# Kernel optimization log

Hardware: AMD Instinct MI355X
Metric: run time of the kernel (lower is better)

The kernel has to match this reference:

```python
import jax, jax.numpy as jnp
import numpy as np

N_NODES = 100000
N_EDGES = 1600000
N_GRAPHS = 64
BN_EPS = 1e-5


def setup_inputs() -> dict:
    key = jax.random.key(0)
    ks = jax.random.split(key, 16)
    inp = {
        'x': jax.random.normal(ks[0], (N_NODES, 768), dtype=jnp.float32),
        'edge_index': jax.random.randint(ks[1], (2, N_EDGES), 0, N_NODES, dtype=jnp.int32),
        'batch': jnp.sort(jax.random.randint(ks[2], (N_NODES,), 0, N_GRAPHS, dtype=jnp.int32)),
        'W_in': jax.random.normal(ks[3], (768, 256), dtype=jnp.float32) * 0.02,
        'b_in': jax.random.normal(ks[4], (256,), dtype=jnp.float32) * 0.02,
        'W_g': jax.random.normal(ks[5], (3, 256, 256), dtype=jnp.float32) * 0.05,
        'b_g': jax.random.normal(ks[6], (3, 256), dtype=jnp.float32) * 0.02,
        'bn_gamma': jax.random.uniform(ks[7], (3, 256), dtype=jnp.float32) + 0.5,
        'bn_beta': jax.random.normal(ks[8], (3, 256), dtype=jnp.float32) * 0.02,
        'bn_mean': jax.random.normal(ks[9], (3, 256), dtype=jnp.float32) * 0.02,
        'bn_var': jax.random.uniform(ks[10], (3, 256), dtype=jnp.float32) + 0.5,
        'W1': jax.random.normal(ks[11], (256, 128), dtype=jnp.float32) * 0.06,
        'b1': jax.random.normal(ks[12], (128,), dtype=jnp.float32) * 0.02,
        'W2': jax.random.normal(ks[13], (128, 128), dtype=jnp.float32) * 0.08,
        'b2': jax.random.normal(ks[14], (128,), dtype=jnp.float32) * 0.02,
    }
    return inp


def reference(x, edge_index, batch, W_in, b_in, W_g, b_g, bn_gamma, bn_beta,
              bn_mean, bn_var, W1, b1, W2, b2):
    N = x.shape[0]
    # Add self loops (PyG GCNConv default)
    loop = jnp.arange(N, dtype=edge_index.dtype)
    src = jnp.concatenate([edge_index[0], loop])  # [E+N]
    dst = jnp.concatenate([edge_index[1], loop])
    # Symmetric GCN normalization: deg over dst after self loops
    deg = jax.ops.segment_sum(jnp.ones_like(src, dtype=x.dtype), dst, num_segments=N)
    dinv = jnp.where(deg > 0, jax.lax.rsqrt(deg), 0.0)
    norm = (dinv[src] * dinv[dst])[:, None]  # [E+N, 1]

    # input projection + relu
    h = jax.nn.relu(x @ W_in + b_in)  # [N, 256]

    for i in range(W_g.shape[0]):
        m = h @ W_g[i]                                   # [N, 256]
        agg = jax.ops.segment_sum(m[src] * norm, dst, num_segments=N) + b_g[i]
        # BatchNorm (eval mode, running stats)
        agg = (agg - bn_mean[i]) * (bn_gamma[i] * jax.lax.rsqrt(bn_var[i] + BN_EPS)) + bn_beta[i]
        h = jax.nn.relu(agg)  # dropout is identity in eval

    # global mean pool per graph
    sums = jax.ops.segment_sum(h, batch, num_segments=N_GRAPHS)       # [G, 256]
    cnts = jax.ops.segment_sum(jnp.ones((N,), x.dtype), batch, num_segments=N_GRAPHS)
    g = sums / jnp.maximum(cnts, 1.0)[:, None]

    # output MLP
    out = jax.nn.relu(g @ W1 + b1) @ W2 + b2  # [G, 128]
    return out
```

## Files before the change

### kernel.cpp

```cpp
#include <hip/hip_runtime.h>
#include <hip/hip_fp16.h>

#define HIDDEN 256

using bfrag = __attribute__((ext_vector_type(8))) short;
using facc4 = __attribute__((ext_vector_type(4))) float;

#define BARRIER_LGKM()                                   \
  do {                                                   \
    asm volatile("s_waitcnt lgkmcnt(0)" ::: "memory");   \
    __builtin_amdgcn_s_barrier();                        \
  } while (0)

__device__ inline short bf16_rne(float x) {
  unsigned u = __builtin_bit_cast(unsigned, x);
  unsigned r = u + 0x7FFFu + ((u >> 16) & 1u);
  return (short)(r >> 16);
}
__device__ inline float bf16_to_f(short h) {
  unsigned u = ((unsigned)(unsigned short)h) << 16;
  return __builtin_bit_cast(float, u);
}
__device__ inline float h2f(unsigned short h) {
  return __half2float(__builtin_bit_cast(__half, h));
}
__device__ inline void cvt8(const float4& a, const float4& b, bfrag& hi, bfrag& lo) {
  float av[8] = {a.x, a.y, a.z, a.w, b.x, b.y, b.z, b.w};
#pragma unroll
  for (int i = 0; i < 8; ++i) {
    unsigned u = __builtin_bit_cast(unsigned, av[i]);
    hi[i] = (short)(u >> 16);
    float r = av[i] - __builtin_bit_cast(float, u & 0xFFFF0000u);
    lo[i] = (short)(__builtin_bit_cast(unsigned, r) >> 16);
  }
}

__global__ __launch_bounds__(256) void k_hist(const int* __restrict__ dst,
                                              int* __restrict__ deg, int E) {
  for (int e = blockIdx.x * blockDim.x + threadIdx.x; e < E;
       e += gridDim.x * blockDim.x)
    atomicAdd(&deg[dst[e]], 1);
}

__global__ __launch_bounds__(256) void k_scan_a(const int* __restrict__ deg,
                                                int* __restrict__ bsum, int N) {
  const int t = threadIdx.x, lane = t & 63, w = t >> 6;
  const int idx = blockIdx.x * 256 + t;
  int x = (idx < N) ? deg[idx] : 0;
#pragma unroll
  for (int off = 32; off >= 1; off >>= 1) x += __shfl_xor(x, off);
  __shared__ int ws[4];
  if (lane == 0) ws[w] = x;
  __syncthreads();
  if (t == 0) bsum[blockIdx.x] = ws[0] + ws[1] + ws[2] + ws[3];
}

__global__ __launch_bounds__(512) void k_scan_b(const int* __restrict__ bsum,
                                                int* __restrict__ boff, int nb) {
  const int t = threadIdx.x, lane = t & 63, w = t >> 6;
  int orig = (t < nb) ? bsum[t] : 0;
  int x = orig;
#pragma unroll
  for (int off = 1; off < 64; off <<= 1) {
    int y = __shfl_up(x, off);
    if (lane >= off) x += y;
  }
  __shared__ int wsum[8];
  if (lane == 63) wsum[w] = x;
  __syncthreads();
  if (w == 0 && lane < 8) {
    int s = wsum[lane];
#pragma unroll
    for (int off = 1; off < 8; off <<= 1) {
      int y = __shfl_up(s, off);
      if (lane >= off) s += y;
    }
    wsum[lane] = s;
  }
  __syncthreads();
  int inc = x + (w > 0 ? wsum[w - 1] : 0);
  if (t < nb) boff[t] = inc - orig;
}

__global__ __launch_bounds__(256) void k_scan_c(const int* __restrict__ deg,
                                                const int* __restrict__ boff,
                                                int* __restrict__ row_ptr,
                                                float* __restrict__ dinv, int N) {
  const int t = threadIdx.x, lane = t & 63, w = t >> 6;
  const int idx = blockIdx.x * 256 + t;
  int d = (idx < N) ? deg[idx] : 0;
  int x = d;
#pragma unroll
  for (int off = 1; off < 64; off <<= 1) {
    int y = __shfl_up(x, off);
    if (lane >= off) x += y;
  }
  __shared__ int ws[4];
  if (lane == 63) ws[w] = x;
  __syncthreads();
  int add = boff[blockIdx.x];
#pragma unroll
  for (int j = 0; j < 4; ++j)
    if (j < w) add += ws[j];
  if (idx < N) {
    row_ptr[idx + 1] = x + add;
    dinv[idx] = 1.0f / sqrtf((float)d + 1.0f);
  }
  if (idx == 0) row_ptr[0] = 0;
}

__global__ __launch_bounds__(256) void k_fill(const int* __restrict__ src,
                                              const int* __restrict__ dst,
                                              const int* __restrict__ row_ptr,
                                              int* __restrict__ fill,
                                              int* __restrict__ csr, int E) {
  for (int e = blockIdx.x * blockDim.x + threadIdx.x; e < E;
       e += gridDim.x * blockDim.x) {
    int d = dst[e];
    int pos = atomicAdd(&fill[d], 1);
    csr[row_ptr[d] + pos] = src[e];
  }
}

__global__ __launch_bounds__(256) void k_prep_w(const float* __restrict__ W_in,
                                                const float* __restrict__ W_g,
                                                short* __restrict__ Wt) {
  const int e = blockIdx.x * blockDim.x + threadIdx.x;
  if (e >= 196608 + 3 * 65536) return;
  float v;
  int k, n;
  size_t base;
  if (e < 196608) {
    k = e >> 8;
    n = e & 255;
    v = W_in[e];
    base = 0;
  } else {
    int r = e - 196608;
    int lyr = r >> 16;
    k = (r >> 8) & 255;
    n = r & 255;
    v = W_g[r];
    base = 393216 + (size_t)lyr * 131072;
  }
  size_t pos = base + (size_t)(k >> 5) * 16384 + (size_t)n * 32 + (k & 31);
  short hi = bf16_rne(v);
  short lo = bf16_rne(v - bf16_to_f(hi));
  Wt[pos] = hi;
  Wt[pos + 8192] = lo;
}

#define MFMA_PASSES(AH, AL, BH, BL)                                        \
  _Pragma("unroll") for (int nf = 0; nf < 4; ++nf)                         \
      _Pragma("unroll") for (int mf = 0; mf < 4; ++mf) acc[mf][nf] =       \
      __builtin_amdgcn_mfma_f32_16x16x32_bf16(AH[mf], BH[nf], acc[mf][nf], \
                                              0, 0, 0);                    \
  _Pragma("unroll") for (int nf = 0; nf < 4; ++nf)                         \
      _Pragma("unroll") for (int mf = 0; mf < 4; ++mf) acc[mf][nf] =       \
      __builtin_amdgcn_mfma_f32_16x16x32_bf16(AH[mf], BL[nf], acc[mf][nf], \
                                              0, 0, 0);                    \
  _Pragma("unroll") for (int nf = 0; nf < 4; ++nf)                         \
      _Pragma("unroll") for (int mf = 0; mf < 4; ++mf) acc[mf][nf] =       \
      __builtin_amdgcn_mfma_f32_16x16x32_bf16(AL[mf], BH[nf], acc[mf][nf], \
                                              0, 0, 0);

template <int EPI>
__global__ __launch_bounds__(256, 2) void gemm_mfma(const float* __restrict__ A,
                                                    const short* __restrict__ Wt,
                                                    const float* __restrict__ aux,
                                                    float* __restrict__ C,
                                                    int M, int K) {
  __shared__ short As[2][64][66];
  const int t = threadIdx.x;
  const int w = t >> 6, l = t & 63;
  const int g = l >> 4, m16 = l & 15;
  const int row0 = blockIdx.x * 64;
  const int arow = t >> 2, ak = (t & 3) << 3;

  facc4 acc[4][4];
#pragma unroll
  for (int i = 0; i < 4; ++i)
#pragma unroll
    for (int j = 0; j < 4; ++j) acc[i][j] = (facc4)(0.0f);

  const int nsteps = K >> 5;
  const int ga = row0 + arow;
  const bool aval = ga < M;
  const float* aptr = A + (size_t)ga * K + ak;
  const short* wbbase = Wt + (size_t)(w * 64 + m16) * 32 + g * 8;

  float4 f0 = make_float4(0.f, 0.f, 0.f, 0.f), f1 = f0;
  if (aval) {
    f0 = *(const float4*)aptr;
    f1 = *(const float4*)(aptr + 4);
  }
  {
    bfrag hi, lo;
    cvt8(f0, f1, hi, lo);
    *(bfrag*)&As[0][arow][ak] = hi;
    *(bfrag*)&As[0][arow][32 + ak] = lo;
  }
  bfrag bh0[4], bl0[4], bh1[4], bl1[4];
#pragma unroll
  for (int nf = 0; nf < 4; ++nf) {
    bh0[nf] = *(const bfrag*)(wbbase + nf * 512);
    bl0[nf] = *(const bfrag*)(wbbase + nf * 512 + 8192);
  }
  if (nsteps > 1 && aval) {
    f0 = *(const float4*)(aptr + 32);
    f1 = *(const float4*)(aptr + 36);
  }

  for (int s = 0; s < nsteps; s += 2) {
    BARRIER_LGKM();
    {
      const short* wb = wbbase + ((size_t)(s + 1) << 14);
#pragma unroll
      for (int nf = 0; nf < 4; ++nf) {
        bh1[nf] = *(const bfrag*)(wb + nf * 512);
        bl1[nf] = *(const bfrag*)(wb + nf * 512 + 8192);
      }
    }
    {
      bfrag ah[4], al[4];
#pragma unroll
      for (int mf = 0; mf < 4; ++mf) {
        ah[mf] = *(const bfrag*)&As[0][mf * 16 + m16][g * 8];
        al[mf] = *(const bfrag*)&As[0][mf * 16 + m16][32 + g * 8];
      }
      MFMA_PASSES(ah, al, bh0, bl0);
    }
    {
      bfrag hi, lo;
      cvt8(f0, f1, hi, lo);
      *(bfrag*)&As[1][arow][ak] = hi;
      *(bfrag*)&As[1][arow][32 + ak] = lo;
    }
    if (s + 2 < nsteps && aval) {
      const float* ap = aptr + (size_t)(s + 2) * 32;
      f0 = *(const float4*)ap;
      f1 = *(const float4*)(ap + 4);
    }
    BARRIER_LGKM();
    if (s + 2 < nsteps) {
      const short* wb = wbbase + ((size_t)(s + 2) << 14);
#pragma unroll
      for (int nf = 0; nf < 4; ++nf) {
        bh0[nf] = *(const bfrag*)(wb + nf * 512);
        bl0[nf] = *(const bfrag*)(wb + nf * 512 + 8192);
      }
    }
    {
      bfrag ah[4], al[4];
#pragma unroll
      for (int mf = 0; mf < 4; ++mf) {
        ah[mf] = *(const bfrag*)&As[1][mf * 16 + m16][g * 8];
        al[mf] = *(const bfrag*)&As[1][mf * 16 + m16][32 + g * 8];
      }
      MFMA_PASSES(ah, al, bh1, bl1);
    }
    if (s + 2 < nsteps) {
      bfrag hi, lo;
      cvt8(f0, f1, hi, lo);
      *(bfrag*)&As[0][arow][ak] = hi;
      *(bfrag*)&As[0][arow][32 + ak] = lo;
      if (s + 3 < nsteps && aval) {
        const float* ap = aptr + (size_t)(s + 3) * 32;
        f0 = *(const float4*)ap;
        f1 = *(const float4*)(ap + 4);
      }
    }
  }
  const int colbase = w * 64;
  if (EPI == 0) {
#pragma unroll
    for (int nf = 0; nf < 4; ++nf) {
      const float bias = aux[colbase + nf * 16 + m16];
#pragma unroll
      for (int mf = 0; mf < 4; ++mf)
#pragma unroll
        for (int r = 0; r < 4; ++r) {
          int row = row0 + mf * 16 + g * 4 + r;
          if (row < M)
            C[(size_t)row * HIDDEN + colbase + nf * 16 + m16] =
                fmaxf(acc[mf][nf][r] + bias, 0.f);
        }
    }
  } else {
    __half* Ch = (__half*)C;
#pragma unroll
    for (int mf = 0; mf < 4; ++mf)
#pragma unroll
      for (int r = 0; r < 4; ++r) {
        int row = row0 + mf * 16 + g * 4 + r;
        if (row >= M) continue;
        const float sc = aux[row];
#pragma unroll
        for (int nf = 0; nf < 4; ++nf)
          Ch[(size_t)row * HIDDEN + colbase + nf * 16 + m16] =
              __float2half(acc[mf][nf][r] * sc);
      }
  }
}

__global__ __launch_bounds__(256) void k_aggregate(
    const unsigned short* __restrict__ mp, const int* __restrict__ row_ptr,
    const int* __restrict__ csr, const float* __restrict__ dinv,
    const float* __restrict__ bg, const float* __restrict__ gamma,
    const float* __restrict__ beta, const float* __restrict__ mean,
    const float* __restrict__ var, float* __restrict__ hout, int N) {
  const int wave = threadIdx.x >> 6, l = threadIdx.x & 63;
  const int v = blockIdx.x * 4 + wave;
  if (v >= N) return;
  const int co = l << 2;
  ushort4 rs = *(const ushort4*)(mp + (size_t)v * HIDDEN + co);
  float4 acc;
  acc.x = h2f(rs.x); acc.y = h2f(rs.y); acc.z = h2f(rs.z); acc.w = h2f(rs.w);
  const int s = row_ptr[v], e = row_ptr[v + 1];
  int i = s;
  for (; i + 8 <= e; i += 8) {
    ushort4 r0 = *(const ushort4*)(mp + (size_t)csr[i + 0] * HIDDEN + co);
    ushort4 r1 = *(const ushort4*)(mp + (size_t)csr[i + 1] * HIDDEN + co);
    ushort4 r2 = *(const ushort4*)(mp + (size_t)csr[i + 2] * HIDDEN + co);
    ushort4 r3 = *(const ushort4*)(mp + (size_t)csr[i + 3] * HIDDEN + co);
    ushort4 r4 = *(const ushort4*)(mp + (size_t)csr[i + 4] * HIDDEN + co);
    ushort4 r5 = *(const ushort4*)(mp + (size_t)csr[i + 5] * HIDDEN + co);
    ushort4 r6 = *(const ushort4*)(mp + (size_t)csr[i + 6] * HIDDEN + co);
    ushort4 r7 = *(const ushort4*)(mp + (size_t)csr[i + 7] * HIDDEN + co);
    acc.x += h2f(r0.x) + h2f(r1.x) + h2f(r2.x) + h2f(r3.x) +
             h2f(r4.x) + h2f(r5.x) + h2f(r6.x) + h2f(r7.x);
    acc.y += h2f(r0.y) + h2f(r1.y) + h2f(r2.y) + h2f(r3.y) +
             h2f(r4.y) + h2f(r5.y) + h2f(r6.y) + h2f(r7.y);
    acc.z += h2f(r0.z) + h2f(r1.z) + h2f(r2.z) + h2f(r3.z) +
             h2f(r4.z) + h2f(r5.z) + h2f(r6.z) + h2f(r7.z);
    acc.w += h2f(r0.w) + h2f(r1.w) + h2f(r2.w) + h2f(r3.w) +
             h2f(r4.w) + h2f(r5.w) + h2f(r6.w) + h2f(r7.w);
  }
  for (; i < e; ++i) {
    ushort4 r0 = *(const ushort4*)(mp + (size_t)csr[i] * HIDDEN + co);
    acc.x += h2f(r0.x);
    acc.y += h2f(r0.y);
    acc.z += h2f(r0.z);
    acc.w += h2f(r0.w);
  }
  const float dv = dinv[v];
  float4 bg4 = *(const float4*)&bg[co];
  float4 g4 = *(const float4*)&gamma[co];
  float4 be4 = *(const float4*)&beta[co];
  float4 mn4 = *(const float4*)&mean[co];
  float4 vr4 = *(const float4*)&var[co];
  float4 o;
  o.x = fmaxf((acc.x * dv + bg4.x - mn4.x) * (g4.x / sqrtf(vr4.x + 1e-5f)) + be4.x, 0.f);
  o.y = fmaxf((acc.y * dv + bg4.y - mn4.y) * (g4.y / sqrtf(vr4.y + 1e-5f)) + be4.y, 0.f);
  o.z = fmaxf((acc.z * dv + bg4.z - mn4.z) * (g4.z / sqrtf(vr4.z + 1e-5f)) + be4.z, 0.f);
  o.w = fmaxf((acc.w * dv + bg4.w - mn4.w) * (g4.w / sqrtf(vr4.w + 1e-5f)) + be4.w, 0.f);
  ((float4*)hout)[(size_t)v * 64 + l] = o;
}

__global__ __launch_bounds__(64) void k_count(const int* __restrict__ batch,
                                              float* __restrict__ cnt, int N,
                                              int G) {
  const int g = threadIdx.x;
  if (g >= G) return;
  int lo = 0, hi = N;
  while (lo < hi) {
    int mid = (lo + hi) >> 1;
    if (batch[mid] < g) lo = mid + 1; else hi = mid;
  }
  int lo2 = lo, hi2 = N;
  while (lo2 < hi2) {
    int mid = (lo2 + hi2) >> 1;
    if (batch[mid] < g + 1) lo2 = mid + 1; else hi2 = mid;
  }
  cnt[g] = (float)(lo2 - lo);
}

__global__ __launch_bounds__(256) void k_pool(const float* __restrict__ h,
                                              const int* __restrict__ batch,
                                              float* __restrict__ sums, int N) {
  const int t = threadIdx.x;
  const int start = blockIdx.x * 256;
  if (start >= N) return;
  const int end = min(start + 256, N);
  float acc = 0.f;
  int cur = batch[start];
  for (int n = start; n < end; ++n) {
    int g = batch[n];
    if (g != cur) {
      atomicAdd(&sums[cur * HIDDEN + t], acc);
      acc = 0.f;
      cur = g;
    }
    acc += h[(size_t)n * HIDDEN + t];
  }
  atomicAdd(&sums[cur * HIDDEN + t], acc);
}

__global__ __launch_bounds__(128) void k_head(const float* __restrict__ sums,
                                              const float* __restrict__ cnt,
                                              const float* __restrict__ W1,
                                              const float* __restrict__ b1,
                                              const float* __restrict__ W2,
                                              const float* __restrict__ b2,
                                              float* __restrict__ out) {
  __shared__ float gr[256];
  __shared__ float t1[128];
  const int b = blockIdx.x, t = threadIdx.x;
  const float inv = 1.0f / fmaxf(cnt[b], 1.0f);
  gr[t] = sums[b * HIDDEN + t] * inv;
  gr[t + 128] = sums[b * HIDDEN + t + 128] * inv;
  __syncthreads();
  float a = b1[t];
  for (int k = 0; k < 256; ++k) a += gr[k] * W1[k * 128 + t];
  t1[t] = fmaxf(a, 0.f);
  __syncthreads();
  float o = b2[t];
  for (int k = 0; k < 128; ++k) o += t1[k] * W2[k * 128 + t];
  out[b * 128 + t] = o;
}

extern "C" void kernel_launch(void* const* d_in, const int* in_sizes, int n_in,
                              void* d_out, int out_size, void* d_ws,
                              size_t ws_size, hipStream_t stream) {
  (void)n_in;
  (void)ws_size;
  const float* x = (const float*)d_in[0];
  const int* ei = (const int*)d_in[1];
  const int* batch = (const int*)d_in[2];
  const float* W_in = (const float*)d_in[3];
  const float* b_in = (const float*)d_in[4];
  const float* W_g = (const float*)d_in[5];
  const float* b_g = (const float*)d_in[6];
  const float* bn_gamma = (const float*)d_in[7];
  const float* bn_beta = (const float*)d_in[8];
  const float* bn_mean = (const float*)d_in[9];
  const float* bn_var = (const float*)d_in[10];
  const float* W1 = (const float*)d_in[11];
  const float* b1 = (const float*)d_in[12];
  const float* W2 = (const float*)d_in[13];
  const float* b2 = (const float*)d_in[14];

  const int KIN = 768;
  const int N = in_sizes[0] / KIN;
  const int E = in_sizes[1] / 2;
  const int G = out_size / 128;

  const int* src = ei;
  const int* dst = ei + E;

  char* ws = (char*)d_ws;
  size_t off = 0;
  auto take = [&](size_t bytes) -> void* {
    void* p = ws + off;
    off += (bytes + 255) & ~(size_t)255;
    return p;
  };
  float* h0 = (float*)take((size_t)N * HIDDEN * 4);
  unsigned short* h1 = (unsigned short*)take((size_t)N * HIDDEN * 2);
  float* dinv = (float*)take((size_t)N * 4);
  int* deg = (int*)take((size_t)N * 4);
  int* fill = (int*)take((size_t)N * 4);
  int* row_ptr = (int*)take((size_t)(N + 1) * 4);
  int* csr = (int*)take((size_t)E * 4);
  float* sums = (float*)take((size_t)G * HIDDEN * 4);
  float* cnt = (float*)take((size_t)G * 4);
  short* Wt = (short*)take((size_t)(393216 + 3 * 131072) * 2);
  const int nb = (N + 255) / 256;
  int* bsum = (int*)take((size_t)nb * 4);
  int* boff = (int*)take((size_t)nb * 4);

  hipMemsetAsync(deg, 0, (size_t)N * 4, stream);
  hipMemsetAsync(fill, 0, (size_t)N * 4, stream);
  hipMemsetAsync(sums, 0, (size_t)G * HIDDEN * 4, stream);

  k_prep_w<<<(196608 + 3 * 65536 + 255) / 256, 256, 0, stream>>>(W_in, W_g, Wt);
  k_hist<<<2048, 256, 0, stream>>>(dst, deg, E);
  k_scan_a<<<nb, 256, 0, stream>>>(deg, bsum, N);
  k_scan_b<<<1, 512, 0, stream>>>(bsum, boff, nb);
  k_scan_c<<<nb, 256, 0, stream>>>(deg, boff, row_ptr, dinv, N);
  k_fill<<<2048, 256, 0, stream>>>(src, dst, row_ptr, fill, csr, E);

  const int gx = (N + 63) / 64;
  gemm_mfma<0><<<gx, 256, 0, stream>>>(x, Wt, b_in, h0, N, KIN);
  for (int i = 0; i < 3; ++i) {
    gemm_mfma<1><<<gx, 256, 0, stream>>>(h0, Wt + 393216 + (size_t)i * 131072,
                                         dinv, (float*)h1, N, HIDDEN);
    k_aggregate<<<(N + 3) / 4, 256, 0, stream>>>(
        h1, row_ptr, csr, dinv, b_g + i * HIDDEN, bn_gamma + i * HIDDEN,
        bn_beta + i * HIDDEN, bn_mean + i * HIDDEN, bn_var + i * HIDDEN, h0, N);
  }
  k_count<<<1, 64, 0, stream>>>(batch, cnt, N, G);
  k_pool<<<(N + 255) / 256, 256, 0, stream>>>(h0, batch, sums, N);
  k_head<<<G, 128, 0, stream>>>(sums, cnt, W1, b1, W2, b2, (float*)d_out);
}
```

Measured before the change: 1.038 ms.

## Switch GEMM to 32x32x16 MFMA tiles with single-buffered weight loads

Rewrites the split-bf16 GEMM inner loop to use 32x32x16 MFMA instructions on 2x2 tiles per wave instead of 16x16x32 on 4x4 fragments. The loop is simplified to one K-step per iteration with a ping-pong LDS index, and weight fragments are loaded each step instead of being prefetched one step ahead. Occupancy hint is raised to 3 blocks per CU. Larger MFMA tiles reduce instruction count and LDS reads per FLOP, but dropping the weight prefetch may expose global load latency.

```diff
diff --git a/kernel.cpp b/kernel.cpp
--- a/kernel.cpp
+++ b/kernel.cpp
@@ -4,7 +4,7 @@
 #define HIDDEN 256
 
 using bfrag = __attribute__((ext_vector_type(8))) short;
-using facc4 = __attribute__((ext_vector_type(4))) float;
+using facc16 = __attribute__((ext_vector_type(16))) float;
 
 #define BARRIER_LGKM()                                   \
   do {                                                   \
@@ -150,22 +150,8 @@
   Wt[pos + 8192] = lo;
 }
 
-#define MFMA_PASSES(AH, AL, BH, BL)                                        \
-  _Pragma("unroll") for (int nf = 0; nf < 4; ++nf)                         \
-      _Pragma("unroll") for (int mf = 0; mf < 4; ++mf) acc[mf][nf] =       \
-      __builtin_amdgcn_mfma_f32_16x16x32_bf16(AH[mf], BH[nf], acc[mf][nf], \
-                                              0, 0, 0);                    \
-  _Pragma("unroll") for (int nf = 0; nf < 4; ++nf)                         \
-      _Pragma("unroll") for (int mf = 0; mf < 4; ++mf) acc[mf][nf] =       \
-      __builtin_amdgcn_mfma_f32_16x16x32_bf16(AH[mf], BL[nf], acc[mf][nf], \
-                                              0, 0, 0);                    \
-  _Pragma("unroll") for (int nf = 0; nf < 4; ++nf)                         \
-      _Pragma("unroll") for (int mf = 0; mf < 4; ++mf) acc[mf][nf] =       \
-      __builtin_amdgcn_mfma_f32_16x16x32_bf16(AL[mf], BH[nf], acc[mf][nf], \
-                                              0, 0, 0);
-
 template <int EPI>
-__global__ __launch_bounds__(256, 2) void gemm_mfma(const float* __restrict__ A,
+__global__ __launch_bounds__(256, 3) void gemm_mfma(const float* __restrict__ A,
                                                     const short* __restrict__ Wt,
                                                     const float* __restrict__ aux,
                                                     float* __restrict__ C,
@@ -173,21 +159,21 @@
   __shared__ short As[2][64][66];
   const int t = threadIdx.x;
   const int w = t >> 6, l = t & 63;
-  const int g = l >> 4, m16 = l & 15;
+  const int g2 = l >> 5, l31 = l & 31;
   const int row0 = blockIdx.x * 64;
+  const int colbase = w * 64;
   const int arow = t >> 2, ak = (t & 3) << 3;
 
-  facc4 acc[4][4];
-#pragma unroll
-  for (int i = 0; i < 4; ++i)
-#pragma unroll
-    for (int j = 0; j < 4; ++j) acc[i][j] = (facc4)(0.0f);
+  facc16 acc[2][2];
+#pragma unroll
+  for (int i = 0; i < 2; ++i)
+#pragma unroll
+    for (int j = 0; j < 2; ++j) acc[i][j] = (facc16)(0.0f);
 
   const int nsteps = K >> 5;
   const int ga = row0 + arow;
   const bool aval = ga < M;
   const float* aptr = A + (size_t)ga * K + ak;
-  const short* wbbase = Wt + (size_t)(w * 64 + m16) * 32 + g * 8;
 
   float4 f0 = make_float4(0.f, 0.f, 0.f, 0.f), f1 = f0;
   if (aval) {
@@ -200,105 +186,91 @@
     *(bfrag*)&As[0][arow][ak] = hi;
     *(bfrag*)&As[0][arow][32 + ak] = lo;
   }
-  bfrag bh0[4], bl0[4], bh1[4], bl1[4];
-#pragma unroll
-  for (int nf = 0; nf < 4; ++nf) {
-    bh0[nf] = *(const bfrag*)(wbbase + nf * 512);
-    bl0[nf] = *(const bfrag*)(wbbase + nf * 512 + 8192);
-  }
   if (nsteps > 1 && aval) {
     f0 = *(const float4*)(aptr + 32);
     f1 = *(const float4*)(aptr + 36);
   }
 
-  for (int s = 0; s < nsteps; s += 2) {
+  int cur = 0;
+  for (int s = 0; s < nsteps; ++s) {
     BARRIER_LGKM();
-    {
-      const short* wb = wbbase + ((size_t)(s + 1) << 14);
-#pragma unroll
-      for (int nf = 0; nf < 4; ++nf) {
-        bh1[nf] = *(const bfrag*)(wb + nf * 512);
-        bl1[nf] = *(const bfrag*)(wb + nf * 512 + 8192);
+    bfrag bh[2][2], bl[2][2];
+#pragma unroll
+    for (int nt = 0; nt < 2; ++nt)
+#pragma unroll
+      for (int kh = 0; kh < 2; ++kh) {
+        const short* wbp = Wt + ((size_t)s << 14) +
+                           (size_t)(colbase + nt * 32 + l31) * 32 + kh * 16 + g2 * 8;
+        bh[nt][kh] = *(const bfrag*)wbp;
+        bl[nt][kh] = *(const bfrag*)(wbp + 8192);
       }
+#pragma unroll
+    for (int kh = 0; kh < 2; ++kh) {
+      bfrag ah[2], al[2];
+#pragma unroll
+      for (int mt = 0; mt < 2; ++mt) {
+        ah[mt] = *(const bfrag*)&As[cur][mt * 32 + l31][kh * 16 + g2 * 8];
+        al[mt] = *(const bfrag*)&As[cur][mt * 32 + l31][32 + kh * 16 + g2 * 8];
+      }
+#pragma unroll
+      for (int mt = 0; mt < 2; ++mt)
+#pragma unroll
+        for (int nt = 0; nt < 2; ++nt)
+          acc[mt][nt] = __builtin_amdgcn_mfma_f32_32x32x16_bf16(
+              ah[mt], bh[nt][kh], acc[mt][nt], 0, 0, 0);
+#pragma unroll
+      for (int mt = 0; mt < 2; ++mt)
+#pragma unroll
+        for (int nt = 0; nt < 2; ++nt)
+          acc[mt][nt] = __builtin_amdgcn_mfma_f32_32x32x16_bf16(
+              ah[mt], bl[nt][kh], acc[mt][nt], 0, 0, 0);
+#pragma unroll
+      for (int mt = 0; mt < 2; ++mt)
+#pragma unroll
+        for (int nt = 0; nt < 2; ++nt)
+          acc[mt][nt] = __builtin_amdgcn_mfma_f32_32x32x16_bf16(
+              al[mt], bh[nt][kh], acc[mt][nt], 0, 0, 0);
     }
-    {
-      bfrag ah[4], al[4];
-#pragma unroll
-      for (int mf = 0; mf < 4; ++mf) {
-        ah[mf] = *(const bfrag*)&As[0][mf * 16 + m16][g * 8];
-        al[mf] = *(const bfrag*)&As[0][mf * 16 + m16][32 + g * 8];
-      }
-      MFMA_PASSES(ah, al, bh0, bl0);
-    }
-    {
+    if (s + 1 < nsteps) {
       bfrag hi, lo;
       cvt8(f0, f1, hi, lo);
-      *(bfrag*)&As[1][arow][ak] = hi;
-      *(bfrag*)&As[1][arow][32 + ak] = lo;
-    }
-    if (s + 2 < nsteps && aval) {
-      const float* ap = aptr + (size_t)(s + 2) * 32;
-      f0 = *(const float4*)ap;
-      f1 = *(const float4*)(ap + 4);
-    }
-    BARRIER_LGKM();
-    if (s + 2 < nsteps) {
-      const short* wb = wbbase + ((size_t)(s + 2) << 14);
-#pragma unroll
-      for (int nf = 0; nf < 4; ++nf) {
-        bh0[nf] = *(const bfrag*)(wb + nf * 512);
-        bl0[nf] = *(const bfrag*)(wb + nf * 512 + 8192);
-      }
-    }
-    {
-      bfrag ah[4], al[4];
-#pragma unroll
-      for (int mf = 0; mf < 4; ++mf) {
-        ah[mf] = *(const bfrag*)&As[1][mf * 16 + m16][g * 8];
-        al[mf] = *(const bfrag*)&As[1][mf * 16 + m16][32 + g * 8];
-      }
-      MFMA_PASSES(ah, al, bh1, bl1);
-    }
-    if (s + 2 < nsteps) {
-      bfrag hi, lo;
-      cvt8(f0, f1, hi, lo);
-      *(bfrag*)&As[0][arow][ak] = hi;
-      *(bfrag*)&As[0][arow][32 + ak] = lo;
-      if (s + 3 < nsteps && aval) {
-        const float* ap = aptr + (size_t)(s + 3) * 32;
+      *(bfrag*)&As[cur ^ 1][arow][ak] = hi;
+      *(bfrag*)&As[cur ^ 1][arow][32 + ak] = lo;
+      if (s + 2 < nsteps && aval) {
+        const float* ap = aptr + (size_t)(s + 2) * 32;
         f0 = *(const float4*)ap;
         f1 = *(const float4*)(ap + 4);
       }
     }
-  }
-  const int colbase = w * 64;
+    cur ^= 1;
+  }
   if (EPI == 0) {
 #pragma unroll
-    for (int nf = 0; nf < 4; ++nf) {
-      const float bias = aux[colbase + nf * 16 + m16];
-#pragma unroll
-      for (int mf = 0; mf < 4; ++mf)
-#pragma unroll
-        for (int r = 0; r < 4; ++r) {
-          int row = row0 + mf * 16 + g * 4 + r;
+    for (int nt = 0; nt < 2; ++nt) {
+      const int col = colbase + nt * 32 + l31;
+      const float bias = aux[col];
+#pragma unroll
+      for (int mt = 0; mt < 2; ++mt)
+#pragma unroll
+        for (int r = 0; r < 16; ++r) {
+          int row = row0 + mt * 32 + (r & 3) + 8 * (r >> 2) + 4 * g2;
           if (row < M)
-            C[(size_t)row * HIDDEN + colbase + nf * 16 + m16] =
-                fmaxf(acc[mf][nf][r] + bias, 0.f);
+            C[(size_t)row * HIDDEN + col] = fmaxf(acc[mt][nt][r] + bias, 0.f);
         }
     }
   } else {
     __half* Ch = (__half*)C;
 #pragma unroll
-    for (int mf = 0; mf < 4; ++mf)
-#pragma unroll
-      for (int r = 0; r < 4; ++r) {
-        int row = row0 + mf * 16 + g * 4 + r;
+    for (int mt = 0; mt < 2; ++mt)
+#pragma unroll
+      for (int r = 0; r < 16; ++r) {
+        int row = row0 + mt * 32 + (r & 3) + 8 * (r >> 2) + 4 * g2;
         if (row >= M) continue;
         const float sc = aux[row];
 #pragma unroll
-        for (int nf = 0; nf < 4; ++nf)
-          Ch[(size_t)row * HIDDEN + colbase + nf * 16 + m16] =
-              __float2half(acc[mf][nf][r] * sc);
+        for (int nt = 0; nt < 2; ++nt)
+          Ch[(size_t)row * HIDDEN + colbase + nt * 32 + l31] =
+              __float2half(acc[mt][nt][r] * sc);
       }
   }
 }
```

Measured after the change: 1.030 ms. About the same (-0.8%).
